# Optimization experiments

Hardware: AMD Instinct MI355X
Metric: run time of the kernel (lower is better)

Reference implementation:

```python
import jax, jax.numpy as jnp
import numpy as np

# T tables, R rows each, dim D; batch B per feature, avg bag size L
T, R, D, B, L = 8, 200_000, 128, 2048, 32
N = T * B * L  # total lookups


def setup_inputs() -> dict:
    key = jax.random.key(0)
    k1, k2, k3, k4, k5 = jax.random.split(key, 5)
    indices = jax.random.randint(k1, (N,), 0, R, dtype=jnp.int32)
    inner = jnp.sort(jax.random.randint(k2, (T * B - 1,), 0, N, dtype=jnp.int32))
    offsets = jnp.concatenate([
        jnp.zeros((1,), jnp.int32), inner, jnp.full((1,), N, jnp.int32)
    ])  # [T*B+1], CSR bag boundaries (feature-major, as in TBE)
    # int8 rowwise-quantized codes, stored as int32 values in [0, 256)
    qweights = jax.random.randint(k3, (T, R, D), 0, 256, dtype=jnp.int32)
    scale = jax.random.uniform(k4, (T, R, 1), jnp.float32) * 0.01
    shift = jax.random.normal(k5, (T, R, 1), jnp.float32) * 0.1
    scale_shift = jnp.concatenate([scale, shift], axis=-1)  # [T, R, 2]
    return {"indices": indices, "offsets": offsets,
            "qweights": qweights, "scale_shift": scale_shift}


def reference(indices, offsets, qweights, scale_shift):
    n = indices.shape[0]
    # bag id for each lookup element from CSR offsets
    seg = jnp.searchsorted(offsets, jnp.arange(n, dtype=offsets.dtype),
                           side="right").astype(jnp.int32) - 1  # [N]
    tbl = seg // B  # table per lookup (identity feature->table map)
    q = qweights[tbl, indices].astype(jnp.float32)          # [N, D] gathered codes
    ss = scale_shift[tbl, indices]                          # [N, 2]
    rows = q * ss[:, :1] + ss[:, 1:]                        # rowwise dequant
    pooled = jax.ops.segment_sum(rows, seg, num_segments=T * B)  # SUM pooling
    # KeyedTensor layout: [B, sum(dims)] = concat of per-feature pooled outputs
    out = pooled.reshape(T, B, D).transpose(1, 0, 2).reshape(B, T * D)
    return out
```

## Files before the change

kernel.cpp:

```cpp
#include <hip/hip_runtime.h>
#include <hip/hip_bf16.h>

constexpr int T = 8;
constexpr int R = 200000;
constexpr int D = 128;
constexpr int B = 2048;
constexpr int NUM_BAGS = T * B;

typedef int iv4 __attribute__((ext_vector_type(4)));
typedef float fv2 __attribute__((ext_vector_type(2)));

__global__ __launch_bounds__(256)
void qembag_kernel(const int* __restrict__ indices,
                   const int* __restrict__ offsets,
                   const int* __restrict__ qweights,
                   const float* __restrict__ scale_shift,
                   float* __restrict__ out) {
    const int wave_id = (int)((blockIdx.x * blockDim.x + threadIdx.x) >> 6);
    if (wave_id >= NUM_BAGS) return;
    const int lane = (int)(threadIdx.x & 63);
    const int half = lane >> 5;
    const int sub  = lane & 31;

    const int bag   = wave_id;
    const int t     = bag >> 11;
    const int batch = bag & (B - 1);

    const int start = offsets[bag];
    const int end   = offsets[bag + 1];
    const int len   = end - start;
    const int C     = len >> 4;

    float acc0 = 0.f, acc1 = 0.f, acc2 = 0.f, acc3 = 0.f;
    float sshift = 0.f;

    const long tbase = (long)t * R;
    const iv4* qw4 = (const iv4*)qweights;
    const fv2* ss2 = (const fv2*)scale_shift;

    int idxb[8];
    if (C > 0) {
#pragma unroll
        for (int k = 0; k < 8; ++k) idxb[k] = indices[start + half + 2 * k];
    }

    for (int c = 0; c < C; ++c) {
        iv4 q[8];
        fv2 s[8];
#pragma unroll
        for (int k = 0; k < 8; ++k) {
            const long r = tbase + idxb[k];
            q[k] = __builtin_nontemporal_load(&qw4[r * 32 + sub]);
            s[k] = ss2[r];
        }

        if (c + 1 < C) {
            const int nbase = start + ((c + 1) << 4) + half;
#pragma unroll
            for (int k = 0; k < 8; ++k) idxb[k] = indices[nbase + 2 * k];
        }

#pragma unroll
        for (int k = 0; k < 8; ++k) {
            const float sc = s[k].x;
            sshift += s[k].y;
            acc0 = fmaf((float)q[k].x, sc, acc0);
            acc1 = fmaf((float)q[k].y, sc, acc1);
            acc2 = fmaf((float)q[k].z, sc, acc2);
            acc3 = fmaf((float)q[k].w, sc, acc3);
        }
    }

    for (int j = start + (C << 4) + half; j < end; j += 2) {
        const long r = tbase + indices[j];
        const iv4 q = __builtin_nontemporal_load(&qw4[r * 32 + sub]);
        const fv2 ss = ss2[r];
        sshift += ss.y;
        acc0 = fmaf((float)q.x, ss.x, acc0);
        acc1 = fmaf((float)q.y, ss.x, acc1);
        acc2 = fmaf((float)q.z, ss.x, acc2);
        acc3 = fmaf((float)q.w, ss.x, acc3);
    }

    acc0 += sshift; acc1 += sshift; acc2 += sshift; acc3 += sshift;

    acc0 += __shfl_down(acc0, 32);
    acc1 += __shfl_down(acc1, 32);
    acc2 += __shfl_down(acc2, 32);
    acc3 += __shfl_down(acc3, 32);

    if (half == 0) {
        float4 v = make_float4(acc0, acc1, acc2, acc3);
        ((float4*)(out + (long)batch * (T * D) + t * D))[sub] = v;
    }
}

extern "C" void kernel_launch(void* const* d_in, const int* in_sizes, int n_in,
                              void* d_out, int out_size, void* d_ws, size_t ws_size,
                              hipStream_t stream) {
    const int*   indices     = (const int*)d_in[0];
    const int*   offsets     = (const int*)d_in[1];
    const int*   qweights    = (const int*)d_in[2];
    const float* scale_shift = (const float*)d_in[3];
    float*       out         = (float*)d_out;

    const int blocks = NUM_BAGS / 4;
    qembag_kernel<<<blocks, 256, 0, stream>>>(indices, offsets, qweights,
                                              scale_shift, out);
}
```

Baseline: 926.5 us.

## Compact touched rows into packed int8 workspace before pooling

Adds a multi-kernel pipeline. A bitmap marks which table rows the indices touch, each touched row is read once and packed from int32 codes into bytes in a workspace copy, and the pooling kernel then gathers those 128-byte packed rows instead of 512-byte int32 rows. The aim is to cut gather traffic for rows that are looked up repeatedly. In exchange it adds three extra launches, full-table bitmap scans, atomics and writes of the packed copy. With mostly-unique random indices, total bytes moved may rise. If the workspace is too small, the old direct kernel is used.

```diff
diff --git a/kernel.cpp b/kernel.cpp
--- a/kernel.cpp
+++ b/kernel.cpp
@@ -1,21 +1,154 @@
 #include <hip/hip_runtime.h>
-#include <hip/hip_bf16.h>
 
 constexpr int T = 8;
 constexpr int R = 200000;
 constexpr int D = 128;
 constexpr int B = 2048;
 constexpr int NUM_BAGS = T * B;
-
-typedef int iv4 __attribute__((ext_vector_type(4)));
+constexpr int ROWS = T * R;
+constexpr int ROW_WORDS = D / 4;
+constexpr long QW8_BYTES = (long)ROWS * D;
+constexpr int BM_WORDS = (ROWS + 31) / 32;
+
+typedef int   iv4 __attribute__((ext_vector_type(4)));
 typedef float fv2 __attribute__((ext_vector_type(2)));
 
 __global__ __launch_bounds__(256)
-void qembag_kernel(const int* __restrict__ indices,
-                   const int* __restrict__ offsets,
-                   const int* __restrict__ qweights,
-                   const float* __restrict__ scale_shift,
-                   float* __restrict__ out) {
+void zero_bitmap_kernel(unsigned* __restrict__ bm) {
+    int i = blockIdx.x * blockDim.x + threadIdx.x;
+    const int stride = gridDim.x * blockDim.x;
+    for (; i < BM_WORDS; i += stride) bm[i] = 0u;
+}
+
+__global__ __launch_bounds__(256)
+void mark_rows_kernel(const int* __restrict__ indices,
+                      const int* __restrict__ offsets,
+                      unsigned* __restrict__ bm) {
+    const int wave = (int)((blockIdx.x * blockDim.x + threadIdx.x) >> 6);
+    if (wave >= NUM_BAGS) return;
+    const int lane = (int)(threadIdx.x & 63);
+    const int t = wave >> 11;
+    const int start = offsets[wave];
+    const int end   = offsets[wave + 1];
+    const int tbase = t * R;
+    for (int j = start + lane; j < end; j += 64) {
+        const unsigned row = (unsigned)(tbase + indices[j]);
+        atomicOr(&bm[row >> 5], 1u << (row & 31));
+    }
+}
+
+__global__ __launch_bounds__(256)
+void compact_rows_kernel(const int* __restrict__ qweights,
+                         const unsigned* __restrict__ bm,
+                         unsigned* __restrict__ qw8) {
+    const int nwaves = (int)((gridDim.x * blockDim.x) >> 6);
+    const int wid    = (int)((blockIdx.x * blockDim.x + threadIdx.x) >> 6);
+    const int lane   = (int)(threadIdx.x & 63);
+    const int half   = lane >> 5;
+    const int sub    = lane & 31;
+    const int npairs = ROWS >> 1;
+    const iv4* qw4 = (const iv4*)qweights;
+    for (int p = wid; p < npairs; p += nwaves) {
+        const int row = 2 * p + half;
+        if (bm[row >> 5] & (1u << (row & 31))) {
+            const iv4 q = __builtin_nontemporal_load(&qw4[(long)row * ROW_WORDS + sub]);
+            const unsigned packed =
+                  ((unsigned)q.x & 255u)
+                | (((unsigned)q.y & 255u) << 8)
+                | (((unsigned)q.z & 255u) << 16)
+                | (((unsigned)q.w & 255u) << 24);
+            qw8[(long)row * ROW_WORDS + sub] = packed;
+        }
+    }
+}
+
+__global__ __launch_bounds__(256)
+void pool_int8_kernel(const int* __restrict__ indices,
+                      const int* __restrict__ offsets,
+                      const unsigned* __restrict__ qw8,
+                      const float* __restrict__ scale_shift,
+                      float* __restrict__ out) {
+    const int wave = (int)((blockIdx.x * blockDim.x + threadIdx.x) >> 6);
+    if (wave >= NUM_BAGS) return;
+    const int lane = (int)(threadIdx.x & 63);
+    const int half = lane >> 5;
+    const int sub  = lane & 31;
+
+    const int t     = wave >> 11;
+    const int batch = wave & (B - 1);
+
+    const int start = offsets[wave];
+    const int end   = offsets[wave + 1];
+    const int len   = end - start;
+    const int C     = len >> 4;
+
+    float acc0 = 0.f, acc1 = 0.f, acc2 = 0.f, acc3 = 0.f;
+    float sshift = 0.f;
+
+    const int tbase = t * R;
+    const fv2* ss2 = (const fv2*)scale_shift;
+
+    int idxb[8];
+    if (C > 0) {
+#pragma unroll
+        for (int k = 0; k < 8; ++k) idxb[k] = indices[start + half + 2 * k];
+    }
+
+    for (int c = 0; c < C; ++c) {
+        unsigned q[8];
+        fv2 s[8];
+#pragma unroll
+        for (int k = 0; k < 8; ++k) {
+            const long r = (long)(tbase + idxb[k]);
+            q[k] = qw8[r * ROW_WORDS + sub];
+            s[k] = ss2[r];
+        }
+        if (c + 1 < C) {
+            const int nbase = start + ((c + 1) << 4) + half;
+#pragma unroll
+            for (int k = 0; k < 8; ++k) idxb[k] = indices[nbase + 2 * k];
+        }
+#pragma unroll
+        for (int k = 0; k < 8; ++k) {
+            const float sc = s[k].x;
+            sshift += s[k].y;
+            acc0 = fmaf((float)( q[k]        & 255u), sc, acc0);
+            acc1 = fmaf((float)((q[k] >>  8) & 255u), sc, acc1);
+            acc2 = fmaf((float)((q[k] >> 16) & 255u), sc, acc2);
+            acc3 = fmaf((float)( q[k] >> 24        ), sc, acc3);
+        }
+    }
+
+    for (int j = start + (C << 4) + half; j < end; j += 2) {
+        const long r = (long)(tbase + indices[j]);
+        const unsigned q = qw8[r * ROW_WORDS + sub];
+        const fv2 ss = ss2[r];
+        sshift += ss.y;
+        acc0 = fmaf((float)( q        & 255u), ss.x, acc0);
+        acc1 = fmaf((float)((q >>  8) & 255u), ss.x, acc1);
+        acc2 = fmaf((float)((q >> 16) & 255u), ss.x, acc2);
+        acc3 = fmaf((float)( q >> 24        ), ss.x, acc3);
+    }
+
+    acc0 += sshift; acc1 += sshift; acc2 += sshift; acc3 += sshift;
+
+    acc0 += __shfl_down(acc0, 32);
+    acc1 += __shfl_down(acc1, 32);
+    acc2 += __shfl_down(acc2, 32);
+    acc3 += __shfl_down(acc3, 32);
+
+    if (half == 0) {
+        float4 v = make_float4(acc0, acc1, acc2, acc3);
+        ((float4*)(out + (long)batch * (T * D) + t * D))[sub] = v;
+    }
+}
+
+__global__ __launch_bounds__(256)
+void qembag_direct_kernel(const int* __restrict__ indices,
+                          const int* __restrict__ offsets,
+                          const int* __restrict__ qweights,
+                          const float* __restrict__ scale_shift,
+                          float* __restrict__ out) {
     const int wave_id = (int)((blockIdx.x * blockDim.x + threadIdx.x) >> 6);
     if (wave_id >= NUM_BAGS) return;
     const int lane = (int)(threadIdx.x & 63);
@@ -53,13 +186,11 @@
             q[k] = __builtin_nontemporal_load(&qw4[r * 32 + sub]);
             s[k] = ss2[r];
         }
-
         if (c + 1 < C) {
             const int nbase = start + ((c + 1) << 4) + half;
 #pragma unroll
             for (int k = 0; k < 8; ++k) idxb[k] = indices[nbase + 2 * k];
         }
-
 #pragma unroll
         for (int k = 0; k < 8; ++k) {
             const float sc = s[k].x;
@@ -104,7 +235,18 @@
     const float* scale_shift = (const float*)d_in[3];
     float*       out         = (float*)d_out;
 
-    const int blocks = NUM_BAGS / 4;
-    qembag_kernel<<<blocks, 256, 0, stream>>>(indices, offsets, qweights,
-                                              scale_shift, out);
-}
+    const size_t need = (size_t)QW8_BYTES + (size_t)BM_WORDS * 4 + 256;
+    if (d_ws != nullptr && ws_size >= need) {
+        unsigned* qw8 = (unsigned*)d_ws;
+        unsigned* bm  = (unsigned*)((char*)d_ws + QW8_BYTES);
+
+        zero_bitmap_kernel<<<64, 256, 0, stream>>>(bm);
+        mark_rows_kernel<<<NUM_BAGS / 4, 256, 0, stream>>>(indices, offsets, bm);
+        compact_rows_kernel<<<8192, 256, 0, stream>>>(qweights, bm, qw8);
+        pool_int8_kernel<<<NUM_BAGS / 4, 256, 0, stream>>>(indices, offsets, qw8,
+                                                           scale_shift, out);
+    } else {
+        qembag_direct_kernel<<<NUM_BAGS / 4, 256, 0, stream>>>(
+            indices, offsets, qweights, scale_shift, out);
+    }
+}
```

After: 1.016 ms. 9.7% more time.
